# Optimization experiments

Measured on AMD Instinct MI355X. Metric: run time of the kernel, lower is better.

Reference implementation:

```python
import jax, jax.numpy as jnp
import numpy as np

EMBED_DIM = 1024
NUM_HEADS = 16
HEAD_DIM = EMBED_DIM // NUM_HEADS
BATCH = 8
SEQ = 1024


def setup_inputs() -> dict:
    key = jax.random.key(0)
    ks = jax.random.split(key, 10)
    s = 1.0 / np.sqrt(EMBED_DIM)
    x = jax.random.normal(ks[0], (BATCH, SEQ, EMBED_DIM), dtype=jnp.float32)
    mask = jax.random.randint(ks[1], (BATCH, SEQ), 0, 2, dtype=jnp.int32)
    mk = lambda k: (jax.random.normal(k, (EMBED_DIM, EMBED_DIM), dtype=jnp.float32) * s)
    return {
        "x": x, "mask": mask,
        "Wq": mk(ks[2]), "bq": jnp.zeros((EMBED_DIM,), jnp.float32),
        "Wk": mk(ks[3]), "bk": jnp.zeros((EMBED_DIM,), jnp.float32),
        "Wv": mk(ks[4]), "bv": jnp.zeros((EMBED_DIM,), jnp.float32),
        "Wo": mk(ks[5]), "bo": jnp.zeros((EMBED_DIM,), jnp.float32),
    }


def _split_heads(t):
    # (B, S, E) -> (B, H, S, D)
    B, S, _ = t.shape
    return t.reshape(B, S, NUM_HEADS, HEAD_DIM).transpose(0, 2, 1, 3)


def reference(x, mask, Wq, bq, Wk, bk, Wv, bv, Wo, bo):
    B, S, E = x.shape
    # torch Linear: y = x @ W.T + b, weight shape (out, in)
    Q = _split_heads(jnp.einsum('bse,oe->bso', x, Wq) + bq)
    K = _split_heads(jnp.einsum('bse,oe->bso', x, Wk) + bk)
    V = _split_heads(jnp.einsum('bse,oe->bso', x, Wv) + bv)
    scores = jnp.einsum('bhqd,bhkd->bhqk', Q, K) / np.sqrt(HEAD_DIM)
    scores = jnp.clip(scores, -50.0, 50.0)
    m = (mask == 0)[:, None, None, :]  # (B,1,1,S)
    scores = jnp.where(m, jnp.float32(-1e9), scores)
    scores = jnp.where(jnp.isfinite(scores), scores, jnp.zeros_like(scores))
    aw = jax.nn.softmax(scores, axis=-1)
    aw = jnp.where(jnp.isfinite(aw), aw, jnp.zeros_like(aw))
    aw = aw / (aw.sum(axis=-1, keepdims=True) + 1e-10)
    # dropout is identity in eval mode
    attended = jnp.einsum('bhqk,bhkd->bhqd', aw, V)
    attended = attended.transpose(0, 2, 1, 3).reshape(B, S, E)
    output = jnp.einsum('bse,oe->bso', attended, Wo) + bo
    return (output, aw)
```

## Files before the change

kernel.cpp:

```cpp
#include <hip/hip_runtime.h>
#include <stdint.h>

typedef _Float16 f16x8 __attribute__((ext_vector_type(8)));
typedef float    f32x4 __attribute__((ext_vector_type(4)));

#define SEQL 1024
#define EMB  1024
#define NH   16
#define HD   64
#define BATCH 8
#define QKVN 3072

__device__ __forceinline__ void gll16(const void* g, void* l) {
  __builtin_amdgcn_global_load_lds(
      (const __attribute__((address_space(1))) unsigned int*)(uintptr_t)g,
      (__attribute__((address_space(3))) unsigned int*)(uintptr_t)l, 16, 0, 0);
}

__device__ __forceinline__ void cvt8(const float* __restrict__ in,
                                     _Float16* __restrict__ out, int i) {
  const float4* p = (const float4*)in;
  float4 a = p[2 * i], b = p[2 * i + 1];
  f16x8 o;
  o[0] = (_Float16)a.x; o[1] = (_Float16)a.y; o[2] = (_Float16)a.z; o[3] = (_Float16)a.w;
  o[4] = (_Float16)b.x; o[5] = (_Float16)b.y; o[6] = (_Float16)b.z; o[7] = (_Float16)b.w;
  ((f16x8*)out)[i] = o;
}

__global__ __launch_bounds__(256) void k_prep(const float* __restrict__ x,
                                              const float* __restrict__ Wq,
                                              const float* __restrict__ Wk,
                                              const float* __restrict__ Wv,
                                              const float* __restrict__ Wo,
                                              const float* __restrict__ bq,
                                              const float* __restrict__ bk,
                                              const float* __restrict__ bv,
                                              _Float16* __restrict__ x16,
                                              _Float16* __restrict__ Wqkv16,
                                              _Float16* __restrict__ Wo16,
                                              float* __restrict__ bqkv) {
  const int bid = blockIdx.x, tid = threadIdx.x;
  if (bid < 4096) {
    cvt8(x, x16, bid * 256 + tid);
  } else if (bid < 4608) {
    cvt8(Wq, Wqkv16, (bid - 4096) * 256 + tid);
  } else if (bid < 5120) {
    cvt8(Wk, Wqkv16 + (size_t)EMB * EMB, (bid - 4608) * 256 + tid);
  } else if (bid < 5632) {
    cvt8(Wv, Wqkv16 + (size_t)2 * EMB * EMB, (bid - 5120) * 256 + tid);
  } else if (bid < 6144) {
    cvt8(Wo, Wo16, (bid - 5632) * 256 + tid);
  } else {
    int i = (bid - 6144) * 256 + tid;
    float v = (i < 1024) ? bq[i] : (i < 2048 ? bk[i - 1024] : bv[i - 2048]);
    bqkv[i] = v;
  }
}

template <int OUT_F16>
__global__ __launch_bounds__(256) void k_gemm_nt(const _Float16* __restrict__ A,
                                                 const _Float16* __restrict__ B,
                                                 const float* __restrict__ bias,
                                                 void* __restrict__ Cv,
                                                 int M, int N, int K) {
  __shared__ __align__(16) _Float16 As[128 * 32];
  __shared__ __align__(16) _Float16 Bs[128 * 32];
  const int nb = N >> 7;
  const int bm = (int)blockIdx.x / nb, bn = (int)blockIdx.x % nb;
  const int m0 = bm << 7, n0 = bn << 7;
  const int tid = threadIdx.x;
  const int wave = tid >> 6, lane = tid & 63, quad = lane >> 4, l16 = lane & 15;
  const int wm = (wave & 1) << 6, wn = (wave >> 1) << 6;

  f32x4 acc[4][4] = {};

  const int c0 = tid, c1 = tid + 256;
  const int row0 = c0 >> 2, ko0 = (c0 & 3) << 3;
  const int row1 = c1 >> 2, ko1 = (c1 & 3) << 3;
  const _Float16* a0 = A + (size_t)(m0 + row0) * K + ko0;
  const _Float16* a1 = A + (size_t)(m0 + row1) * K + ko1;
  const _Float16* b0 = B + (size_t)(n0 + row0) * K + ko0;
  const _Float16* b1 = B + (size_t)(n0 + row1) * K + ko1;

  for (int k0 = 0; k0 < K; k0 += 32) {
    __syncthreads();
    gll16(a0 + k0, As + (size_t)c0 * 8);
    gll16(a1 + k0, As + (size_t)c1 * 8);
    gll16(b0 + k0, Bs + (size_t)c0 * 8);
    gll16(b1 + k0, Bs + (size_t)c1 * 8);
    __syncthreads();

    f16x8 af[4], bf[4];
#pragma unroll
    for (int i = 0; i < 4; ++i)
      af[i] = *(const f16x8*)(As + ((wm + (i << 4) + l16) << 5) + (quad << 3));
#pragma unroll
    for (int i = 0; i < 4; ++i)
      bf[i] = *(const f16x8*)(Bs + ((wn + (i << 4) + l16) << 5) + (quad << 3));
#pragma unroll
    for (int i = 0; i < 4; ++i)
#pragma unroll
      for (int j = 0; j < 4; ++j)
        acc[i][j] = __builtin_amdgcn_mfma_f32_16x16x32_f16(af[i], bf[j], acc[i][j], 0, 0, 0);
  }

#pragma unroll
  for (int j = 0; j < 4; ++j) {
    int col = n0 + wn + (j << 4) + l16;
    float bb = bias[col];
#pragma unroll
    for (int i = 0; i < 4; ++i) {
      int rowb = m0 + wm + (i << 4) + (quad << 2);
#pragma unroll
      for (int r = 0; r < 4; ++r) {
        float v = acc[i][j][r] + bb;
        if (OUT_F16)
          ((_Float16*)Cv)[(size_t)(rowb + r) * N + col] = (_Float16)v;
        else
          ((float*)Cv)[(size_t)(rowb + r) * N + col] = v;
      }
    }
  }
}

__global__ __launch_bounds__(256) void k_transpose_v(const _Float16* __restrict__ QKV,
                                                     _Float16* __restrict__ Vt) {
  int tid = blockIdx.x * 256 + threadIdx.x;
  int d = tid & 63;
  int s0 = ((tid >> 6) & 127) << 3;
  int h = (tid >> 13) & 15;
  int b = tid >> 17;
  const _Float16* src = QKV + ((size_t)(b * SEQL + s0)) * QKVN + 2048 + h * HD + d;
  f16x8 t;
#pragma unroll
  for (int j = 0; j < 8; ++j) t[j] = src[(size_t)j * QKVN];
  *(f16x8*)(Vt + ((size_t)((b * NH + h) * HD + d)) * SEQL + s0) = t;
}

#define PPAD 272
#define OPAD 68

__global__ __launch_bounds__(256) void k_attn_fused(const _Float16* __restrict__ QKV,
                                                    const _Float16* __restrict__ Vt,
                                                    const int* __restrict__ mask,
                                                    float* __restrict__ aw,
                                                    _Float16* __restrict__ att) {
  __shared__ __align__(16) _Float16 pbuf[4][16 * PPAD];
  __shared__ float obuf[4][16 * OPAD];
  __shared__ float sm[4][16], sl[4][16];

  const int qt = blockIdx.x, h = blockIdx.y, b = blockIdx.z;
  const int tid = threadIdx.x;
  const int wave = tid >> 6, lane = tid & 63, quad = lane >> 4, l16 = lane & 15;

  const _Float16* Qbase =
      QKV + ((size_t)(b * SEQL + qt * 16 + l16)) * QKVN + h * HD + quad * 8;
  f16x8 qf0 = *(const f16x8*)(Qbase);
  f16x8 qf1 = *(const f16x8*)(Qbase + 32);

  float p[16][4];
  float mr[4], lr[4];
#pragma unroll
  for (int r = 0; r < 4; ++r) mr[r] = -3.0e38f;

  const int* mrow = mask + b * SEQL;
  const _Float16* Kb0 = QKV + (size_t)b * SEQL * QKVN + 1024 + h * HD + quad * 8;

#pragma unroll
  for (int ct = 0; ct < 16; ++ct) {
    int col = wave * 256 + ct * 16 + l16;
    const _Float16* Kb = Kb0 + (size_t)col * QKVN;
    f16x8 kf0 = *(const f16x8*)(Kb);
    f16x8 kf1 = *(const f16x8*)(Kb + 32);
    f32x4 acc = {};
    acc = __builtin_amdgcn_mfma_f32_16x16x32_f16(qf0, kf0, acc, 0, 0, 0);
    acc = __builtin_amdgcn_mfma_f32_16x16x32_f16(qf1, kf1, acc, 0, 0, 0);
    bool mk = (mrow[col] == 0);
#pragma unroll
    for (int r = 0; r < 4; ++r) {
      float s = acc[r] * 0.125f;
      s = fminf(fmaxf(s, -50.f), 50.f);
      if (mk) s = -1.0e9f;
      p[ct][r] = s;
      mr[r] = fmaxf(mr[r], s);
    }
  }

#pragma unroll
  for (int r = 0; r < 4; ++r) {
    float m = mr[r];
    m = fmaxf(m, __shfl_xor(m, 1, 16));
    m = fmaxf(m, __shfl_xor(m, 2, 16));
    m = fmaxf(m, __shfl_xor(m, 4, 16));
    m = fmaxf(m, __shfl_xor(m, 8, 16));
    mr[r] = m;
  }
#pragma unroll
  for (int r = 0; r < 4; ++r) lr[r] = 0.f;
#pragma unroll
  for (int ct = 0; ct < 16; ++ct) {
#pragma unroll
    for (int r = 0; r < 4; ++r) {
      float e = __expf(p[ct][r] - mr[r]);
      p[ct][r] = e;
      lr[r] += e;
    }
  }
#pragma unroll
  for (int r = 0; r < 4; ++r) {
    float l = lr[r];
    l += __shfl_xor(l, 1, 16);
    l += __shfl_xor(l, 2, 16);
    l += __shfl_xor(l, 4, 16);
    l += __shfl_xor(l, 8, 16);
    lr[r] = l;
  }
  if (l16 == 0) {
#pragma unroll
    for (int r = 0; r < 4; ++r) {
      sm[wave][quad * 4 + r] = mr[r];
      sl[wave][quad * 4 + r] = lr[r];
    }
  }
  __syncthreads();

  float f[4];
#pragma unroll
  for (int r = 0; r < 4; ++r) {
    int row = quad * 4 + r;
    float M = fmaxf(fmaxf(sm[0][row], sm[1][row]), fmaxf(sm[2][row], sm[3][row]));
    float L = sl[0][row] * __expf(sm[0][row] - M) + sl[1][row] * __expf(sm[1][row] - M) +
              sl[2][row] * __expf(sm[2][row] - M) + sl[3][row] * __expf(sm[3][row] - M);
    f[r] = __expf(mr[r] - M) / L;
  }

  float* awb = aw + (((size_t)(b * NH + h)) * SEQL + qt * 16) * SEQL;
  _Float16* pw = pbuf[wave];
#pragma unroll
  for (int ct = 0; ct < 16; ++ct) {
#pragma unroll
    for (int r = 0; r < 4; ++r) {
      float v = p[ct][r] * f[r];
      awb[(size_t)(quad * 4 + r) * SEQL + wave * 256 + ct * 16 + l16] = v;
      pw[(quad * 4 + r) * PPAD + ct * 16 + l16] = (_Float16)v;
    }
  }

  f32x4 opv[4] = {};
  const _Float16* vtb =
      Vt + ((size_t)(b * NH + h)) * HD * SEQL + wave * 256 + quad * 8;
#pragma unroll
  for (int k = 0; k < 256; k += 32) {
    f16x8 af = *(const f16x8*)(pw + l16 * PPAD + k + quad * 8);
#pragma unroll
    for (int nt = 0; nt < 4; ++nt) {
      f16x8 bf = *(const f16x8*)(vtb + (size_t)(nt * 16 + l16) * SEQL + k);
      opv[nt] = __builtin_amdgcn_mfma_f32_16x16x32_f16(af, bf, opv[nt], 0, 0, 0);
    }
  }

#pragma unroll
  for (int nt = 0; nt < 4; ++nt)
#pragma unroll
    for (int r = 0; r < 4; ++r)
      obuf[wave][(quad * 4 + r) * OPAD + nt * 16 + l16] = opv[nt][r];
  __syncthreads();

  {
    int col = tid & 63;
    int r0 = tid >> 6;
#pragma unroll
    for (int i = 0; i < 4; ++i) {
      int row = r0 + i * 4;
      float o = obuf[0][row * OPAD + col] + obuf[1][row * OPAD + col] +
                obuf[2][row * OPAD + col] + obuf[3][row * OPAD + col];
      att[((size_t)(b * SEQL + qt * 16 + row)) * EMB + h * HD + col] = (_Float16)o;
    }
  }
}

extern "C" void kernel_launch(void* const* d_in, const int* in_sizes, int n_in,
                              void* d_out, int out_size, void* d_ws, size_t ws_size,
                              hipStream_t stream) {
  const float* x  = (const float*)d_in[0];
  const int* mask = (const int*)d_in[1];
  const float* Wq = (const float*)d_in[2];
  const float* bq = (const float*)d_in[3];
  const float* Wk = (const float*)d_in[4];
  const float* bk = (const float*)d_in[5];
  const float* Wv = (const float*)d_in[6];
  const float* bv = (const float*)d_in[7];
  const float* Wo = (const float*)d_in[8];
  const float* bo = (const float*)d_in[9];

  float* out = (float*)d_out;
  float* aw = out + (size_t)BATCH * SEQL * EMB;

  char* ws = (char*)d_ws;
  _Float16* x16    = (_Float16*)(ws);
  _Float16* Wqkv16 = (_Float16*)(ws + ((size_t)16 << 20));
  _Float16* Wo16   = (_Float16*)(ws + ((size_t)22 << 20));
  float*    bqkv   = (float*)   (ws + ((size_t)24 << 20));
  _Float16* QKV16  = (_Float16*)(ws + ((size_t)25 << 20));
  _Float16* Vt16   = (_Float16*)(ws + ((size_t)73 << 20));
  _Float16* att16  = (_Float16*)(ws + ((size_t)89 << 20));

  const int M = BATCH * SEQL;

  k_prep<<<6156, 256, 0, stream>>>(x, Wq, Wk, Wv, Wo, bq, bk, bv,
                                   x16, Wqkv16, Wo16, bqkv);

  k_gemm_nt<1><<<(M / 128) * (QKVN / 128), 256, 0, stream>>>(x16, Wqkv16, bqkv, QKV16,
                                                             M, QKVN, EMB);

  k_transpose_v<<<4096, 256, 0, stream>>>(QKV16, Vt16);

  k_attn_fused<<<dim3(SEQL / 16, NH, BATCH), 256, 0, stream>>>(QKV16, Vt16, mask, aw, att16);

  k_gemm_nt<0><<<(M / 128) * (EMB / 128), 256, 0, stream>>>(att16, Wo16, bo, out,
                                                            M, EMB, EMB);
}
```

Before: 914.3 us.

## Stage K and V tiles through swizzled LDS with global_load_lds in fused attention

After: 912.8 us. Within noise of the previous version (-0.2%).

```diff
diff --git a/kernel.cpp b/kernel.cpp
--- a/kernel.cpp
+++ b/kernel.cpp
@@ -140,13 +140,20 @@
 #define PPAD 272
 #define OPAD 68
 
+__device__ __forceinline__ void stage_v(const _Float16* __restrict__ Vme,
+                                        _Float16* __restrict__ dst, int c) {
+#pragma unroll
+  for (int it = 0; it < 8; ++it)
+    gll16(Vme + (size_t)it * 8 * SEQL + (size_t)c * 256, dst + (size_t)it * 2048);
+}
+
 __global__ __launch_bounds__(256) void k_attn_fused(const _Float16* __restrict__ QKV,
                                                     const _Float16* __restrict__ Vt,
                                                     const int* __restrict__ mask,
                                                     float* __restrict__ aw,
                                                     _Float16* __restrict__ att) {
+  __shared__ __align__(16) _Float16 ubuf[16384];
   __shared__ __align__(16) _Float16 pbuf[4][16 * PPAD];
-  __shared__ float obuf[4][16 * OPAD];
   __shared__ float sm[4][16], sl[4][16];
 
   const int qt = blockIdx.x, h = blockIdx.y, b = blockIdx.z;
@@ -164,25 +171,43 @@
   for (int r = 0; r < 4; ++r) mr[r] = -3.0e38f;
 
   const int* mrow = mask + b * SEQL;
-  const _Float16* Kb0 = QKV + (size_t)b * SEQL * QKVN + 1024 + h * HD + quad * 8;
-
-#pragma unroll
-  for (int ct = 0; ct < 16; ++ct) {
-    int col = wave * 256 + ct * 16 + l16;
-    const _Float16* Kb = Kb0 + (size_t)col * QKVN;
-    f16x8 kf0 = *(const f16x8*)(Kb);
-    f16x8 kf1 = *(const f16x8*)(Kb + 32);
-    f32x4 acc = {};
-    acc = __builtin_amdgcn_mfma_f32_16x16x32_f16(qf0, kf0, acc, 0, 0, 0);
-    acc = __builtin_amdgcn_mfma_f32_16x16x32_f16(qf1, kf1, acc, 0, 0, 0);
-    bool mk = (mrow[col] == 0);
-#pragma unroll
-    for (int r = 0; r < 4; ++r) {
-      float s = acc[r] * 0.125f;
-      s = fminf(fmaxf(s, -50.f), 50.f);
-      if (mk) s = -1.0e9f;
-      p[ct][r] = s;
-      mr[r] = fmaxf(mr[r], s);
+
+  const _Float16* Kg = QKV + (size_t)b * SEQL * QKVN + 1024 + h * HD;
+  const int krow = tid >> 3;
+  const int kdch = (tid & 7) ^ (krow & 7);
+  const _Float16* Kme = Kg + (size_t)krow * QKVN + kdch * 8;
+  const _Float16* Vg = Vt + ((size_t)(b * NH + h)) * HD * SEQL;
+  const int vrow = tid >> 5;
+  const int vsch = (tid & 31) ^ (vrow & 7);
+  const _Float16* Vme = Vg + (size_t)vrow * SEQL + vsch * 8;
+  _Float16* kdst = ubuf + (size_t)tid * 8;
+
+  for (int c = 0; c < 4; ++c) {
+    if (c) __syncthreads();
+#pragma unroll
+    for (int it = 0; it < 8; ++it)
+      gll16(Kme + (size_t)(c * 256 + it * 32) * QKVN, kdst + (size_t)it * 2048);
+    __syncthreads();
+#pragma unroll
+    for (int ctw = 0; ctw < 4; ++ctw) {
+      int sloc = wave * 64 + ctw * 16 + l16;
+      int ch0 = sloc * 8 + (quad ^ (sloc & 7));
+      f16x8 kf0 = *(const f16x8*)(ubuf + (size_t)ch0 * 8);
+      f16x8 kf1 = *(const f16x8*)(ubuf + (size_t)(ch0 ^ 4) * 8);
+      f32x4 acc = {};
+      acc = __builtin_amdgcn_mfma_f32_16x16x32_f16(qf0, kf0, acc, 0, 0, 0);
+      acc = __builtin_amdgcn_mfma_f32_16x16x32_f16(qf1, kf1, acc, 0, 0, 0);
+      int col = c * 256 + sloc;
+      bool mk = (mrow[col] == 0);
+      int pidx = c * 4 + ctw;
+#pragma unroll
+      for (int r = 0; r < 4; ++r) {
+        float s = acc[r] * 0.125f;
+        s = fminf(fmaxf(s, -50.f), 50.f);
+        if (mk) s = -1.0e9f;
+        p[pidx][r] = s;
+        mr[r] = fmaxf(mr[r], s);
+      }
     }
   }
 
@@ -198,11 +223,11 @@
 #pragma unroll
   for (int r = 0; r < 4; ++r) lr[r] = 0.f;
 #pragma unroll
-  for (int ct = 0; ct < 16; ++ct) {
+  for (int pidx = 0; pidx < 16; ++pidx) {
 #pragma unroll
     for (int r = 0; r < 4; ++r) {
-      float e = __expf(p[ct][r] - mr[r]);
-      p[ct][r] = e;
+      float e = __expf(p[pidx][r] - mr[r]);
+      p[pidx][r] = e;
       lr[r] += e;
     }
   }
@@ -224,6 +249,8 @@
   }
   __syncthreads();
 
+  stage_v(Vme, kdst, 0);
+
   float f[4];
 #pragma unroll
   for (int r = 0; r < 4; ++r) {
@@ -237,33 +264,45 @@
   float* awb = aw + (((size_t)(b * NH + h)) * SEQL + qt * 16) * SEQL;
   _Float16* pw = pbuf[wave];
 #pragma unroll
-  for (int ct = 0; ct < 16; ++ct) {
+  for (int pidx = 0; pidx < 16; ++pidx) {
+    int col = ((pidx >> 2) << 8) + (wave << 6) + ((pidx & 3) << 4) + l16;
 #pragma unroll
     for (int r = 0; r < 4; ++r) {
-      float v = p[ct][r] * f[r];
-      awb[(size_t)(quad * 4 + r) * SEQL + wave * 256 + ct * 16 + l16] = v;
-      pw[(quad * 4 + r) * PPAD + ct * 16 + l16] = (_Float16)v;
+      float v = p[pidx][r] * f[r];
+      awb[(size_t)(quad * 4 + r) * SEQL + col] = v;
+      pw[(quad * 4 + r) * PPAD + pidx * 16 + l16] = (_Float16)v;
     }
   }
 
   f32x4 opv[4] = {};
-  const _Float16* vtb =
-      Vt + ((size_t)(b * NH + h)) * HD * SEQL + wave * 256 + quad * 8;
-#pragma unroll
-  for (int k = 0; k < 256; k += 32) {
-    f16x8 af = *(const f16x8*)(pw + l16 * PPAD + k + quad * 8);
-#pragma unroll
-    for (int nt = 0; nt < 4; ++nt) {
-      f16x8 bf = *(const f16x8*)(vtb + (size_t)(nt * 16 + l16) * SEQL + k);
-      opv[nt] = __builtin_amdgcn_mfma_f32_16x16x32_f16(af, bf, opv[nt], 0, 0, 0);
-    }
-  }
-
+  for (int c = 0; c < 4; ++c) {
+    __syncthreads();
+#pragma unroll
+    for (int ks = 0; ks < 2; ++ks) {
+      int klocal = c * 64 + ks * 32;
+      f16x8 af = *(const f16x8*)(pw + l16 * PPAD + klocal + quad * 8);
+#pragma unroll
+      for (int nt = 0; nt < 4; ++nt) {
+        int d = nt * 16 + l16;
+        int sch = wave * 8 + ks * 4 + quad;
+        int ch = d * 32 + (sch ^ (d & 7));
+        f16x8 bf = *(const f16x8*)(ubuf + (size_t)ch * 8);
+        opv[nt] = __builtin_amdgcn_mfma_f32_16x16x32_f16(af, bf, opv[nt], 0, 0, 0);
+      }
+    }
+    if (c < 3) {
+      __syncthreads();
+      stage_v(Vme, kdst, c + 1);
+    }
+  }
+  __syncthreads();
+
+  float* ob = (float*)ubuf;
 #pragma unroll
   for (int nt = 0; nt < 4; ++nt)
 #pragma unroll
     for (int r = 0; r < 4; ++r)
-      obuf[wave][(quad * 4 + r) * OPAD + nt * 16 + l16] = opv[nt][r];
+      ob[(wave * 16 + quad * 4 + r) * OPAD + nt * 16 + l16] = opv[nt][r];
   __syncthreads();
 
   {
@@ -272,8 +311,8 @@
 #pragma unroll
     for (int i = 0; i < 4; ++i) {
       int row = r0 + i * 4;
-      float o = obuf[0][row * OPAD + col] + obuf[1][row * OPAD + col] +
-                obuf[2][row * OPAD + col] + obuf[3][row * OPAD + col];
+      float o = ob[row * OPAD + col] + ob[(16 + row) * OPAD + col] +
+                ob[(32 + row) * OPAD + col] + ob[(48 + row) * OPAD + col];
       att[((size_t)(b * SEQL + qt * 16 + row)) * EMB + h * HD + col] = (_Float16)o;
     }
   }
```
